# Kernel optimization log

Hardware: AMD Instinct MI355X
Metric: run time of the kernel (lower is better)

Reference implementation:

```python
import jax, jax.numpy as jnp
import numpy as np

B, NQ, C, H, W, HEADS = 8, 300, 256, 64, 64, 8
HD = C // HEADS
SCALING = float(HD) ** (-0.5)


def setup_inputs() -> dict:
    key = jax.random.key(0)
    ks = jax.random.split(key, 12)
    pts = jax.random.uniform(ks[3], (B, NQ, 2), jnp.float32)
    pts = pts * jnp.array([W - 1, H - 1], jnp.float32)  # (x, y) in pixel coords
    s = 1.0 / np.sqrt(C)
    return {
        "query": jax.random.normal(ks[0], (B, NQ, C), jnp.float32),
        "key": jax.random.normal(ks[1], (B, C, H, W), jnp.float32),
        "value": jax.random.normal(ks[2], (B, C, H, W), jnp.float32),
        "sampling_points": pts,
        "Wq": jax.random.normal(ks[4], (C, C), jnp.float32) * s,
        "bq": jnp.zeros((C,), jnp.float32),
        "Wk": jax.random.normal(ks[5], (C, C), jnp.float32) * s,
        "bk": jnp.zeros((C,), jnp.float32),
        "Wv": jax.random.normal(ks[6], (C, C), jnp.float32) * s,
        "bv": jnp.zeros((C,), jnp.float32),
        "Wo": jax.random.normal(ks[7], (C, C), jnp.float32) * s,
        "bo": jnp.zeros((C,), jnp.float32),
    }


def _sample_rows(feat, y):
    # feat: [b,heads,hd,h,w]; y: [b,q] float row coordinate.
    # Returns feat linearly interpolated in y for every column: [b,q,heads,hd,w]
    h = feat.shape[3]
    y0f = jnp.clip(jnp.floor(y), 0.0, h - 1)
    wy = y - y0f
    y0 = y0f.astype(jnp.int32)
    y1 = jnp.clip(y0 + 1, 0, h - 1)
    g = jax.vmap(lambda f, idx: f[:, :, idx, :])  # per-batch -> [heads,hd,q,w]
    r = g(feat, y0) * (1.0 - wy)[:, None, None, :, None] + g(feat, y1) * wy[:, None, None, :, None]
    return jnp.transpose(r, (0, 3, 1, 2, 4))


def _sample_cols(feat, x):
    # feat: [b,heads,hd,h,w]; x: [b,q] float col coordinate -> [b,q,heads,hd,h]
    w = feat.shape[4]
    x0f = jnp.clip(jnp.floor(x), 0.0, w - 1)
    wx = x - x0f
    x0 = x0f.astype(jnp.int32)
    x1 = jnp.clip(x0 + 1, 0, w - 1)
    g = jax.vmap(lambda f, idx: f[:, :, :, idx])  # per-batch -> [heads,hd,h,q]
    c = g(feat, x0) * (1.0 - wx)[:, None, None, None, :] + g(feat, x1) * wx[:, None, None, None, :]
    return jnp.transpose(c, (0, 4, 1, 2, 3))


def reference(query, key, value, sampling_points, Wq, bq, Wk, bk, Wv, bv, Wo, bo):
    b, nq, c = query.shape
    h, w = key.shape[2], key.shape[3]
    pq = (query @ Wq.T + bq) * SCALING                     # [b,nq,C]
    pk = jnp.einsum('oc,bchw->bohw', Wk, key) + bk[None, :, None, None]
    pv = jnp.einsum('oc,bchw->bohw', Wv, value) + bv[None, :, None, None]
    pq = pq.reshape(b, nq, HEADS, HD)
    pk = pk.reshape(b, HEADS, HD, h, w)
    pv = pv.reshape(b, HEADS, HD, h, w)
    x, y = sampling_points[..., 0], sampling_points[..., 1]
    # criss-cross weights: row through y (w samples) + column through x (h samples)
    k_row = _sample_rows(pk, y)                            # [b,q,heads,hd,w]
    k_col = _sample_cols(pk, x)                            # [b,q,heads,hd,h]
    w_row = jnp.einsum('bqnd,bqndw->bqnw', pq, k_row)
    w_col = jnp.einsum('bqnd,bqndk->bqnk', pq, k_col)
    attn = jax.nn.softmax(jnp.concatenate([w_row, w_col], axis=-1), axis=-1)
    a_row, a_col = attn[..., :w], attn[..., w:]
    v_row = _sample_rows(pv, y)
    v_col = _sample_cols(pv, x)
    out = jnp.einsum('bqnw,bqndw->bqnd', a_row, v_row) + jnp.einsum('bqnk,bqndk->bqnd', a_col, v_col)
    out = out.reshape(b, nq, c)
    return out @ Wo.T + bo
```

## Files before the change

kernel.cpp:

```cpp
#include <hip/hip_runtime.h>
#include <hip/hip_bf16.h>
#include <math.h>

constexpr int cB = 8, cNQ = 300, cC = 256, cH = 64, cW = 64, cHEADS = 8, cHD = 32;
constexpr int cHW = cH * cW;
constexpr int cM = cB * cNQ;
constexpr float cSCALE = 0.1767766952966369f;

typedef __bf16 bf16_t;
typedef bf16_t bf16x4 __attribute__((ext_vector_type(4)));
typedef bf16_t bf16x8 __attribute__((ext_vector_type(8)));
typedef float f32x4 __attribute__((ext_vector_type(4)));
typedef _Float16 f16_t;
typedef f16_t f16x8 __attribute__((ext_vector_type(8)));

__global__ __launch_bounds__(256) void proj_mfma_k(
    const float* __restrict__ X, const float* __restrict__ Wt,
    const float* __restrict__ bias, float* __restrict__ out,
    float scale, int M) {
  __shared__ bf16_t Xs[128 * 64];
  __shared__ bf16_t Ws[64 * 64];
  int m0 = blockIdx.x * 128;
  int o0 = blockIdx.y * 64;
  int tid = threadIdx.x;
  int lane = tid & 63, w = tid >> 6;
  int moff = (w & 1) * 64, ooff = (w >> 1) * 32;
  int l15 = lane & 15, l4 = lane >> 4;
  int srow = tid >> 1;
  int schalf = (tid & 1) * 32;
  int wo_l = tid >> 2;
  int wcg = (tid & 3) * 16;

  f32x4 acc[4][2];
#pragma unroll
  for (int m = 0; m < 4; ++m)
#pragma unroll
    for (int n = 0; n < 2; ++n) acc[m][n] = (f32x4){0.f, 0.f, 0.f, 0.f};

  for (int c0 = 0; c0 < cC; c0 += 64) {
    {
      int mrow = min(m0 + srow, M - 1);
      const float4* xr = (const float4*)(X + (size_t)mrow * cC + c0 + schalf);
      int sw = (srow & 7) * 8;
#pragma unroll
      for (int i = 0; i < 4; ++i) {
        float4 a = xr[i * 2], b4 = xr[i * 2 + 1];
        bf16x8 v = {(bf16_t)a.x, (bf16_t)a.y, (bf16_t)a.z, (bf16_t)a.w,
                    (bf16_t)b4.x, (bf16_t)b4.y, (bf16_t)b4.z, (bf16_t)b4.w};
        *(bf16x8*)&Xs[srow * 64 + ((schalf + i * 8) ^ sw)] = v;
      }
    }
    {
      const float4* wr = (const float4*)(Wt + (size_t)(o0 + wo_l) * cC + c0 + wcg);
      float4 a = wr[0], b4 = wr[1], c4 = wr[2], d4 = wr[3];
      bf16x8 w0 = {(bf16_t)a.x, (bf16_t)a.y, (bf16_t)a.z, (bf16_t)a.w,
                   (bf16_t)b4.x, (bf16_t)b4.y, (bf16_t)b4.z, (bf16_t)b4.w};
      bf16x8 w1 = {(bf16_t)c4.x, (bf16_t)c4.y, (bf16_t)c4.z, (bf16_t)c4.w,
                   (bf16_t)d4.x, (bf16_t)d4.y, (bf16_t)d4.z, (bf16_t)d4.w};
      int sw = (wo_l & 7) * 8;
      *(bf16x8*)&Ws[wo_l * 64 + (wcg ^ sw)] = w0;
      *(bf16x8*)&Ws[wo_l * 64 + ((wcg + 8) ^ sw)] = w1;
    }
    __syncthreads();
#pragma unroll
    for (int s = 0; s < 2; ++s) {
      int c8 = s * 32 + l4 * 8;
      bf16x8 afr[4], bfr[2];
#pragma unroll
      for (int m = 0; m < 4; ++m) {
        int r = moff + m * 16 + l15;
        afr[m] = *(const bf16x8*)&Xs[r * 64 + (c8 ^ ((r & 7) * 8))];
      }
#pragma unroll
      for (int n = 0; n < 2; ++n) {
        int r = ooff + n * 16 + l15;
        bfr[n] = *(const bf16x8*)&Ws[r * 64 + (c8 ^ ((r & 7) * 8))];
      }
#pragma unroll
      for (int m = 0; m < 4; ++m)
#pragma unroll
        for (int n = 0; n < 2; ++n)
          acc[m][n] = __builtin_amdgcn_mfma_f32_16x16x32_bf16(
              afr[m], bfr[n], acc[m][n], 0, 0, 0);
    }
    __syncthreads();
  }

  float b0 = bias[o0 + ooff + l15];
  float b1 = bias[o0 + ooff + 16 + l15];
#pragma unroll
  for (int m = 0; m < 4; ++m) {
    int mr = m0 + moff + m * 16 + l4 * 4;
#pragma unroll
    for (int reg = 0; reg < 4; ++reg) {
      if (mr + reg < M) {
        out[(size_t)(mr + reg) * cC + o0 + ooff + l15] =
            (acc[m][0][reg] + b0) * scale;
        out[(size_t)(mr + reg) * cC + o0 + ooff + 16 + l15] =
            (acc[m][1][reg] + b1) * scale;
      }
    }
  }
}

__global__ __launch_bounds__(256) void proj_kv_mfma_k(
    const float* __restrict__ key, const float* __restrict__ value,
    const float* __restrict__ Wk, const float* __restrict__ bk,
    const float* __restrict__ Wv, const float* __restrict__ bv,
    f16_t* __restrict__ pkT, f16_t* __restrict__ pvT,
    f16_t* __restrict__ pkTc, f16_t* __restrict__ pvTc) {
  int z = blockIdx.z;
  int b = z >> 1;
  bool isv = z & 1;
  const float* X = (isv ? value : key) + (size_t)b * cC * cHW;
  const float* Wm = isv ? Wv : Wk;
  const float* bb = isv ? bv : bk;
  f16_t* outT = (isv ? pvT : pkT) + (size_t)b * cHEADS * cHW * cHD;
  f16_t* outTc = (isv ? pvTc : pkTc) + (size_t)b * cHEADS * cHW * cHD;
  int hw0 = blockIdx.x * 128;
  int o0 = blockIdx.y * 64;

  __shared__ bf16_t Xs[128 * 64];
  __shared__ bf16_t Ws[64 * 64];

  int tid = threadIdx.x;
  int lane = tid & 63, w = tid >> 6;
  int hwl = (w & 1) * 64 + lane;
  int cbase = (w >> 1) * 32;
  int wo_l = tid >> 2;
  int wcg = (tid & 3) * 16;
  int hwoff = (w & 1) * 64, ooff = (w >> 1) * 32;
  int l15 = lane & 15, l4 = lane >> 4;

  f32x4 acc[4][2];
#pragma unroll
  for (int m = 0; m < 4; ++m)
#pragma unroll
    for (int n = 0; n < 2; ++n) acc[m][n] = (f32x4){0.f, 0.f, 0.f, 0.f};

  for (int c0 = 0; c0 < cC; c0 += 64) {
    const float* xcol = X + (size_t)(c0 + cbase) * cHW + hw0 + hwl;
#pragma unroll
    for (int i = 0; i < 8; ++i) {
      float f0 = xcol[(size_t)(i * 4 + 0) * cHW];
      float f1 = xcol[(size_t)(i * 4 + 1) * cHW];
      float f2 = xcol[(size_t)(i * 4 + 2) * cHW];
      float f3 = xcol[(size_t)(i * 4 + 3) * cHW];
      bf16x4 v = {(bf16_t)f0, (bf16_t)f1, (bf16_t)f2, (bf16_t)f3};
      int c_l = cbase + i * 4;
      *(bf16x4*)&Xs[hwl * 64 + (c_l ^ ((hwl & 7) * 8))] = v;
    }
    {
      const float4* wrow = (const float4*)(Wm + (size_t)(o0 + wo_l) * cC + c0 + wcg);
      float4 a = wrow[0], b4 = wrow[1], c4 = wrow[2], d4 = wrow[3];
      bf16x8 w0 = {(bf16_t)a.x, (bf16_t)a.y, (bf16_t)a.z, (bf16_t)a.w,
                   (bf16_t)b4.x, (bf16_t)b4.y, (bf16_t)b4.z, (bf16_t)b4.w};
      bf16x8 w1 = {(bf16_t)c4.x, (bf16_t)c4.y, (bf16_t)c4.z, (bf16_t)c4.w,
                   (bf16_t)d4.x, (bf16_t)d4.y, (bf16_t)d4.z, (bf16_t)d4.w};
      int sw = (wo_l & 7) * 8;
      *(bf16x8*)&Ws[wo_l * 64 + (wcg ^ sw)] = w0;
      *(bf16x8*)&Ws[wo_l * 64 + ((wcg + 8) ^ sw)] = w1;
    }
    __syncthreads();
#pragma unroll
    for (int s = 0; s < 2; ++s) {
      int c8 = s * 32 + l4 * 8;
      bf16x8 afr[4], bfr[2];
#pragma unroll
      for (int m = 0; m < 4; ++m) {
        int r = hwoff + m * 16 + l15;
        afr[m] = *(const bf16x8*)&Xs[r * 64 + (c8 ^ ((r & 7) * 8))];
      }
#pragma unroll
      for (int n = 0; n < 2; ++n) {
        int r = ooff + n * 16 + l15;
        bfr[n] = *(const bf16x8*)&Ws[r * 64 + (c8 ^ ((r & 7) * 8))];
      }
#pragma unroll
      for (int m = 0; m < 4; ++m)
#pragma unroll
        for (int n = 0; n < 2; ++n)
          acc[m][n] = __builtin_amdgcn_mfma_f32_16x16x32_bf16(
              afr[m], bfr[n], acc[m][n], 0, 0, 0);
    }
    __syncthreads();
  }

  int head = (o0 + ooff) >> 5;
  f16_t* obase = outT + (size_t)head * cHW * cHD;
  f16_t* obaseC = outTc + (size_t)head * cHW * cHD;
  float bias0 = bb[o0 + ooff + l15];
  float bias1 = bb[o0 + ooff + 16 + l15];
#pragma unroll
  for (int m = 0; m < 4; ++m) {
    int hwr = hwoff + m * 16 + l4 * 4;
#pragma unroll
    for (int reg = 0; reg < 4; ++reg) {
      int hw = hw0 + hwr + reg;
      f16_t v0 = (f16_t)(acc[m][0][reg] + bias0);
      f16_t v1 = (f16_t)(acc[m][1][reg] + bias1);
      size_t rowoff = (size_t)hw * cHD;
      obase[rowoff + l15] = v0;
      obase[rowoff + 16 + l15] = v1;
      int yy = hw >> 6, xx = hw & 63;
      size_t rowoffC = (size_t)(xx * cH + yy) * cHD;
      obaseC[rowoffC + l15] = v0;
      obaseC[rowoffC + 16 + l15] = v1;
    }
  }
}

__global__ __launch_bounds__(256) void attn_k(
    const float* __restrict__ pq, const f16_t* __restrict__ pkT,
    const f16_t* __restrict__ pkTc, const f16_t* __restrict__ pvT,
    const f16_t* __restrict__ pvTc, const float* __restrict__ pts,
    float* __restrict__ out) {
  int bid = blockIdx.x;
  int xcd = bid & 7;
  int t = bid >> 3;
  int phase = t / 150;
  int idx = t - phase * 150;
  int g = xcd + 8 * phase;
  int b = g >> 2;
  int hp = g & 3;
  int lane = threadIdx.x & 63;
  int wid = threadIdx.x >> 6;
  int n = hp * 2 + (wid & 1);
  int q = idx * 2 + (wid >> 1);

  float x = pts[((size_t)b * cNQ + q) * 2 + 0];
  float y = pts[((size_t)b * cNQ + q) * 2 + 1];
  float y0f = fminf(fmaxf(floorf(y), 0.f), (float)(cH - 1));
  float x0f = fminf(fmaxf(floorf(x), 0.f), (float)(cW - 1));
  float wy = y - y0f, wx = x - x0f;
  int y0 = (int)y0f, y1 = min(y0 + 1, cH - 1);
  int x0 = (int)x0f, x1 = min(x0 + 1, cW - 1);

  size_t hoff = (size_t)(b * cHEADS + n) * cHW * cHD;
  const f16_t* kTb = pkT + hoff;
  const f16_t* kTcb = pkTc + hoff;
  const f16_t* vTb = pvT + hoff;
  const f16_t* vTcb = pvTc + hoff;

  int g16 = lane >> 2, ch = lane & 3;
  f16x8 vr0[4], vr1[4], vc0[4], vc1[4];
#pragma unroll
  for (int k = 0; k < 4; ++k) {
    int p = g16 * 4 + k;
    vr0[k] = *(const f16x8*)(vTb + (size_t)(y0 * cW + p) * cHD + ch * 8);
    vr1[k] = *(const f16x8*)(vTb + (size_t)(y1 * cW + p) * cHD + ch * 8);
    vc0[k] = *(const f16x8*)(vTcb + (size_t)(x0 * cH + p) * cHD + ch * 8);
    vc1[k] = *(const f16x8*)(vTcb + (size_t)(x1 * cH + p) * cHD + ch * 8);
  }

  const f16x8* kr0 = (const f16x8*)(kTb + (size_t)(y0 * cW + lane) * cHD);
  const f16x8* kr1 = (const f16x8*)(kTb + (size_t)(y1 * cW + lane) * cHD);
  const f16x8* kc0 = (const f16x8*)(kTcb + (size_t)(x0 * cH + lane) * cHD);
  const f16x8* kc1 = (const f16x8*)(kTcb + (size_t)(x1 * cH + lane) * cHD);
  const float4* qb = (const float4*)(pq + ((size_t)b * cNQ + q) * cC + n * cHD);
  float wr0 = 0.f, wr1 = 0.f, wc0 = 0.f, wc1 = 0.f;
#pragma unroll
  for (int c = 0; c < 4; ++c) {
    f16x8 a0 = kr0[c], a1 = kr1[c], b0 = kc0[c], b1 = kc1[c];
    float4 q0 = qb[c * 2], q1 = qb[c * 2 + 1];
    float qs[8] = {q0.x, q0.y, q0.z, q0.w, q1.x, q1.y, q1.z, q1.w};
#pragma unroll
    for (int j = 0; j < 8; ++j) {
      float f0 = (float)a0[j], f1 = (float)a1[j];
      float h0 = (float)b0[j], h1 = (float)b1[j];
      if (j & 1) {
        wr1 += qs[j] * (f0 + wy * (f1 - f0));
        wc1 += qs[j] * (h0 + wx * (h1 - h0));
      } else {
        wr0 += qs[j] * (f0 + wy * (f1 - f0));
        wc0 += qs[j] * (h0 + wx * (h1 - h0));
      }
    }
  }
  float wrow = wr0 + wr1, wcol = wc0 + wc1;

  float m = fmaxf(wrow, wcol);
#pragma unroll
  for (int s = 32; s > 0; s >>= 1) m = fmaxf(m, __shfl_xor(m, s, 64));
  float er = expf(wrow - m), ec = expf(wcol - m);
  float ssum = er + ec;
#pragma unroll
  for (int s = 32; s > 0; s >>= 1) ssum += __shfl_xor(ssum, s, 64);

  float acc[8];
#pragma unroll
  for (int j = 0; j < 8; ++j) acc[j] = 0.f;
#pragma unroll
  for (int k = 0; k < 4; ++k) {
    int p = g16 * 4 + k;
    float ar = __shfl(er, p, 64);
    float ac = __shfl(ec, p, 64);
#pragma unroll
    for (int j = 0; j < 8; ++j) {
      float r0 = (float)vr0[k][j], r1 = (float)vr1[k][j];
      float c0 = (float)vc0[k][j], c1 = (float)vc1[k][j];
      acc[j] += ar * (r0 + wy * (r1 - r0)) + ac * (c0 + wx * (c1 - c0));
    }
  }
#pragma unroll
  for (int s = 4; s <= 32; s <<= 1)
#pragma unroll
    for (int j = 0; j < 8; ++j) acc[j] += __shfl_xor(acc[j], s, 64);

  float inv = 1.f / ssum;
  if (lane < 4) {
    float* op = out + ((size_t)b * cNQ + q) * cC + n * cHD + ch * 8;
    float4 o0 = {acc[0] * inv, acc[1] * inv, acc[2] * inv, acc[3] * inv};
    float4 o1 = {acc[4] * inv, acc[5] * inv, acc[6] * inv, acc[7] * inv};
    *(float4*)op = o0;
    *(float4*)(op + 4) = o1;
  }
}

extern "C" void kernel_launch(void* const* d_in, const int* in_sizes, int n_in,
                              void* d_out, int out_size, void* d_ws, size_t ws_size,
                              hipStream_t stream) {
  const float* query = (const float*)d_in[0];
  const float* key   = (const float*)d_in[1];
  const float* value = (const float*)d_in[2];
  const float* pts   = (const float*)d_in[3];
  const float* Wq = (const float*)d_in[4];
  const float* bq = (const float*)d_in[5];
  const float* Wk = (const float*)d_in[6];
  const float* bk = (const float*)d_in[7];
  const float* Wv = (const float*)d_in[8];
  const float* bv = (const float*)d_in[9];
  const float* Wo = (const float*)d_in[10];
  const float* bo = (const float*)d_in[11];
  float* out = (float*)d_out;

  const size_t kvsz = (size_t)cB * cC * cHW;
  float* pq = (float*)d_ws;
  f16_t* pkT = (f16_t*)(pq + (size_t)cM * cC);
  f16_t* pvT = pkT + kvsz;
  f16_t* pkTc = pvT + kvsz;
  f16_t* pvTc = pkTc + kvsz;
  float* ao = (float*)(pvTc + kvsz);

  proj_mfma_k<<<dim3((cM + 127) / 128, cC / 64), 256, 0, stream>>>(
      query, Wq, bq, pq, cSCALE, cM);
  proj_kv_mfma_k<<<dim3(cHW / 128, cC / 64, cB * 2), 256, 0, stream>>>(
      key, value, Wk, bk, Wv, bv, pkT, pvT, pkTc, pvTc);
  attn_k<<<cB * cNQ * 2, 256, 0, stream>>>(pq, pkT, pkTc, pvT, pvTc, pts, ao);
  proj_mfma_k<<<dim3((cM + 127) / 128, cC / 64), 256, 0, stream>>>(
      ao, Wo, bo, out, 1.0f, cM);
}
```

Measured before the change: 105.4 us.

## Load activations straight into MFMA fragments with register double-buffering

Both projection GEMM kernels stop staging activation tiles in LDS. Each lane now loads its own fp32 activation fragment from global memory directly into registers, converts it to bf16 and feeds it to MFMA, with two register buffers so the next k-step load overlaps the current MFMAs. Weights are pre-packed once per block into LDS in fragment order, which removes the per-k-step barriers. The cost is more registers and uncoalesced, strided global loads in the key/value kernel (16 lanes per channel row).

Measured after the change: 124.2 us. 17.8% more time.

```diff
diff --git a/kernel.cpp b/kernel.cpp
--- a/kernel.cpp
+++ b/kernel.cpp
@@ -8,7 +8,6 @@
 constexpr float cSCALE = 0.1767766952966369f;
 
 typedef __bf16 bf16_t;
-typedef bf16_t bf16x4 __attribute__((ext_vector_type(4)));
 typedef bf16_t bf16x8 __attribute__((ext_vector_type(8)));
 typedef float f32x4 __attribute__((ext_vector_type(4)));
 typedef _Float16 f16_t;
@@ -18,18 +17,33 @@
     const float* __restrict__ X, const float* __restrict__ Wt,
     const float* __restrict__ bias, float* __restrict__ out,
     float scale, int M) {
-  __shared__ bf16_t Xs[128 * 64];
-  __shared__ bf16_t Ws[64 * 64];
+  __shared__ bf16_t Wf[8 * 4 * 64 * 8];
   int m0 = blockIdx.x * 128;
   int o0 = blockIdx.y * 64;
   int tid = threadIdx.x;
   int lane = tid & 63, w = tid >> 6;
-  int moff = (w & 1) * 64, ooff = (w >> 1) * 32;
   int l15 = lane & 15, l4 = lane >> 4;
-  int srow = tid >> 1;
-  int schalf = (tid & 1) * 32;
-  int wo_l = tid >> 2;
-  int wcg = (tid & 3) * 16;
+
+  {
+    int ntile = tid >> 6;
+    int o = o0 + ntile * 16 + l15;
+    const float* wsrc = Wt + (size_t)o * cC + l4 * 8;
+#pragma unroll
+    for (int s = 0; s < 8; ++s) {
+      float4 f0 = *(const float4*)(wsrc + s * 32);
+      float4 f1 = *(const float4*)(wsrc + s * 32 + 4);
+      bf16x8 v = {(bf16_t)f0.x, (bf16_t)f0.y, (bf16_t)f0.z, (bf16_t)f0.w,
+                  (bf16_t)f1.x, (bf16_t)f1.y, (bf16_t)f1.z, (bf16_t)f1.w};
+      *(bf16x8*)&Wf[(size_t)((s * 4 + ntile) * 64 + lane) * 8] = v;
+    }
+  }
+  __syncthreads();
+
+  int moff = (w & 1) * 64;
+  int nbase = (w >> 1) * 2;
+  int mrow[4];
+#pragma unroll
+  for (int m = 0; m < 4; ++m) mrow[m] = min(m0 + moff + m * 16 + l15, M - 1);
 
   f32x4 acc[4][2];
 #pragma unroll
@@ -37,66 +51,51 @@
 #pragma unroll
     for (int n = 0; n < 2; ++n) acc[m][n] = (f32x4){0.f, 0.f, 0.f, 0.f};
 
-  for (int c0 = 0; c0 < cC; c0 += 64) {
-    {
-      int mrow = min(m0 + srow, M - 1);
-      const float4* xr = (const float4*)(X + (size_t)mrow * cC + c0 + schalf);
-      int sw = (srow & 7) * 8;
-#pragma unroll
-      for (int i = 0; i < 4; ++i) {
-        float4 a = xr[i * 2], b4 = xr[i * 2 + 1];
-        bf16x8 v = {(bf16_t)a.x, (bf16_t)a.y, (bf16_t)a.z, (bf16_t)a.w,
-                    (bf16_t)b4.x, (bf16_t)b4.y, (bf16_t)b4.z, (bf16_t)b4.w};
-        *(bf16x8*)&Xs[srow * 64 + ((schalf + i * 8) ^ sw)] = v;
-      }
-    }
-    {
-      const float4* wr = (const float4*)(Wt + (size_t)(o0 + wo_l) * cC + c0 + wcg);
-      float4 a = wr[0], b4 = wr[1], c4 = wr[2], d4 = wr[3];
-      bf16x8 w0 = {(bf16_t)a.x, (bf16_t)a.y, (bf16_t)a.z, (bf16_t)a.w,
-                   (bf16_t)b4.x, (bf16_t)b4.y, (bf16_t)b4.z, (bf16_t)b4.w};
-      bf16x8 w1 = {(bf16_t)c4.x, (bf16_t)c4.y, (bf16_t)c4.z, (bf16_t)c4.w,
-                   (bf16_t)d4.x, (bf16_t)d4.y, (bf16_t)d4.z, (bf16_t)d4.w};
-      int sw = (wo_l & 7) * 8;
-      *(bf16x8*)&Ws[wo_l * 64 + (wcg ^ sw)] = w0;
-      *(bf16x8*)&Ws[wo_l * 64 + ((wcg + 8) ^ sw)] = w1;
-    }
-    __syncthreads();
-#pragma unroll
-    for (int s = 0; s < 2; ++s) {
-      int c8 = s * 32 + l4 * 8;
-      bf16x8 afr[4], bfr[2];
-#pragma unroll
-      for (int m = 0; m < 4; ++m) {
-        int r = moff + m * 16 + l15;
-        afr[m] = *(const bf16x8*)&Xs[r * 64 + (c8 ^ ((r & 7) * 8))];
-      }
-#pragma unroll
-      for (int n = 0; n < 2; ++n) {
-        int r = ooff + n * 16 + l15;
-        bfr[n] = *(const bf16x8*)&Ws[r * 64 + (c8 ^ ((r & 7) * 8))];
-      }
-#pragma unroll
-      for (int m = 0; m < 4; ++m)
-#pragma unroll
-        for (int n = 0; n < 2; ++n)
-          acc[m][n] = __builtin_amdgcn_mfma_f32_16x16x32_bf16(
-              afr[m], bfr[n], acc[m][n], 0, 0, 0);
-    }
-    __syncthreads();
-  }
-
-  float b0 = bias[o0 + ooff + l15];
-  float b1 = bias[o0 + ooff + 16 + l15];
+  float4 fa[4][2], fb[4][2];
+  auto loadx = [&](float4 F[4][2], int s) {
+#pragma unroll
+    for (int m = 0; m < 4; ++m) {
+      const float4* xr = (const float4*)(X + (size_t)mrow[m] * cC + s * 32 + l4 * 8);
+      F[m][0] = xr[0];
+      F[m][1] = xr[1];
+    }
+  };
+  auto consume = [&](float4 F[4][2], int s) {
+    bf16x8 b0 = *(const bf16x8*)&Wf[(size_t)((s * 4 + nbase) * 64 + lane) * 8];
+    bf16x8 b1 = *(const bf16x8*)&Wf[(size_t)((s * 4 + nbase + 1) * 64 + lane) * 8];
+#pragma unroll
+    for (int m = 0; m < 4; ++m) {
+      float4 x0 = F[m][0], x1 = F[m][1];
+      bf16x8 a = {(bf16_t)x0.x, (bf16_t)x0.y, (bf16_t)x0.z, (bf16_t)x0.w,
+                  (bf16_t)x1.x, (bf16_t)x1.y, (bf16_t)x1.z, (bf16_t)x1.w};
+      acc[m][0] = __builtin_amdgcn_mfma_f32_16x16x32_bf16(a, b0, acc[m][0], 0, 0, 0);
+      acc[m][1] = __builtin_amdgcn_mfma_f32_16x16x32_bf16(a, b1, acc[m][1], 0, 0, 0);
+    }
+  };
+
+  loadx(fa, 0);
+#pragma unroll
+  for (int s = 0; s < 8; ++s) {
+    if (s & 1) {
+      if (s < 7) loadx(fa, s + 1);
+      consume(fb, s);
+    } else {
+      if (s < 7) loadx(fb, s + 1);
+      consume(fa, s);
+    }
+  }
+
+  float b0 = bias[o0 + nbase * 16 + l15];
+  float b1 = bias[o0 + nbase * 16 + 16 + l15];
 #pragma unroll
   for (int m = 0; m < 4; ++m) {
     int mr = m0 + moff + m * 16 + l4 * 4;
 #pragma unroll
     for (int reg = 0; reg < 4; ++reg) {
       if (mr + reg < M) {
-        out[(size_t)(mr + reg) * cC + o0 + ooff + l15] =
+        out[(size_t)(mr + reg) * cC + o0 + nbase * 16 + l15] =
             (acc[m][0][reg] + b0) * scale;
-        out[(size_t)(mr + reg) * cC + o0 + ooff + 16 + l15] =
+        out[(size_t)(mr + reg) * cC + o0 + nbase * 16 + 16 + l15] =
             (acc[m][1][reg] + b1) * scale;
       }
     }
@@ -120,77 +119,75 @@
   int hw0 = blockIdx.x * 128;
   int o0 = blockIdx.y * 64;
 
-  __shared__ bf16_t Xs[128 * 64];
-  __shared__ bf16_t Ws[64 * 64];
-
+  __shared__ bf16_t Wf[8 * 4 * 64 * 8];
   int tid = threadIdx.x;
   int lane = tid & 63, w = tid >> 6;
-  int hwl = (w & 1) * 64 + lane;
-  int cbase = (w >> 1) * 32;
-  int wo_l = tid >> 2;
-  int wcg = (tid & 3) * 16;
-  int hwoff = (w & 1) * 64, ooff = (w >> 1) * 32;
   int l15 = lane & 15, l4 = lane >> 4;
 
+  {
+    int ntile = tid >> 6;
+    int o = o0 + ntile * 16 + l15;
+    const float* wsrc = Wm + (size_t)o * cC + l4 * 8;
+#pragma unroll
+    for (int s = 0; s < 8; ++s) {
+      float4 f0 = *(const float4*)(wsrc + s * 32);
+      float4 f1 = *(const float4*)(wsrc + s * 32 + 4);
+      bf16x8 v = {(bf16_t)f0.x, (bf16_t)f0.y, (bf16_t)f0.z, (bf16_t)f0.w,
+                  (bf16_t)f1.x, (bf16_t)f1.y, (bf16_t)f1.z, (bf16_t)f1.w};
+      *(bf16x8*)&Wf[(size_t)((s * 4 + ntile) * 64 + lane) * 8] = v;
+    }
+  }
+  __syncthreads();
+
+  int hwoff = (w & 1) * 64;
+  int nbase = (w >> 1) * 2;
+  const float* xb = X + hw0 + hwoff + l15;
+
   f32x4 acc[4][2];
 #pragma unroll
   for (int m = 0; m < 4; ++m)
 #pragma unroll
     for (int n = 0; n < 2; ++n) acc[m][n] = (f32x4){0.f, 0.f, 0.f, 0.f};
 
-  for (int c0 = 0; c0 < cC; c0 += 64) {
-    const float* xcol = X + (size_t)(c0 + cbase) * cHW + hw0 + hwl;
-#pragma unroll
-    for (int i = 0; i < 8; ++i) {
-      float f0 = xcol[(size_t)(i * 4 + 0) * cHW];
-      float f1 = xcol[(size_t)(i * 4 + 1) * cHW];
-      float f2 = xcol[(size_t)(i * 4 + 2) * cHW];
-      float f3 = xcol[(size_t)(i * 4 + 3) * cHW];
-      bf16x4 v = {(bf16_t)f0, (bf16_t)f1, (bf16_t)f2, (bf16_t)f3};
-      int c_l = cbase + i * 4;
-      *(bf16x4*)&Xs[hwl * 64 + (c_l ^ ((hwl & 7) * 8))] = v;
-    }
-    {
-      const float4* wrow = (const float4*)(Wm + (size_t)(o0 + wo_l) * cC + c0 + wcg);
-      float4 a = wrow[0], b4 = wrow[1], c4 = wrow[2], d4 = wrow[3];
-      bf16x8 w0 = {(bf16_t)a.x, (bf16_t)a.y, (bf16_t)a.z, (bf16_t)a.w,
-                   (bf16_t)b4.x, (bf16_t)b4.y, (bf16_t)b4.z, (bf16_t)b4.w};
-      bf16x8 w1 = {(bf16_t)c4.x, (bf16_t)c4.y, (bf16_t)c4.z, (bf16_t)c4.w,
-                   (bf16_t)d4.x, (bf16_t)d4.y, (bf16_t)d4.z, (bf16_t)d4.w};
-      int sw = (wo_l & 7) * 8;
-      *(bf16x8*)&Ws[wo_l * 64 + (wcg ^ sw)] = w0;
-      *(bf16x8*)&Ws[wo_l * 64 + ((wcg + 8) ^ sw)] = w1;
-    }
-    __syncthreads();
-#pragma unroll
-    for (int s = 0; s < 2; ++s) {
-      int c8 = s * 32 + l4 * 8;
-      bf16x8 afr[4], bfr[2];
-#pragma unroll
-      for (int m = 0; m < 4; ++m) {
-        int r = hwoff + m * 16 + l15;
-        afr[m] = *(const bf16x8*)&Xs[r * 64 + (c8 ^ ((r & 7) * 8))];
-      }
-#pragma unroll
-      for (int n = 0; n < 2; ++n) {
-        int r = ooff + n * 16 + l15;
-        bfr[n] = *(const bf16x8*)&Ws[r * 64 + (c8 ^ ((r & 7) * 8))];
-      }
-#pragma unroll
-      for (int m = 0; m < 4; ++m)
-#pragma unroll
-        for (int n = 0; n < 2; ++n)
-          acc[m][n] = __builtin_amdgcn_mfma_f32_16x16x32_bf16(
-              afr[m], bfr[n], acc[m][n], 0, 0, 0);
-    }
-    __syncthreads();
-  }
-
-  int head = (o0 + ooff) >> 5;
+  float fa[4][8], fb[4][8];
+  auto loadx = [&](float F[4][8], int s) {
+    const float* xc = xb + (size_t)(s * 32 + l4 * 8) * cHW;
+#pragma unroll
+    for (int m = 0; m < 4; ++m)
+#pragma unroll
+      for (int j = 0; j < 8; ++j)
+        F[m][j] = xc[(size_t)j * cHW + m * 16];
+  };
+  auto consume = [&](float F[4][8], int s) {
+    bf16x8 b0 = *(const bf16x8*)&Wf[(size_t)((s * 4 + nbase) * 64 + lane) * 8];
+    bf16x8 b1 = *(const bf16x8*)&Wf[(size_t)((s * 4 + nbase + 1) * 64 + lane) * 8];
+#pragma unroll
+    for (int m = 0; m < 4; ++m) {
+      bf16x8 a = {(bf16_t)F[m][0], (bf16_t)F[m][1], (bf16_t)F[m][2],
+                  (bf16_t)F[m][3], (bf16_t)F[m][4], (bf16_t)F[m][5],
+                  (bf16_t)F[m][6], (bf16_t)F[m][7]};
+      acc[m][0] = __builtin_amdgcn_mfma_f32_16x16x32_bf16(a, b0, acc[m][0], 0, 0, 0);
+      acc[m][1] = __builtin_amdgcn_mfma_f32_16x16x32_bf16(a, b1, acc[m][1], 0, 0, 0);
+    }
+  };
+
+  loadx(fa, 0);
+#pragma unroll
+  for (int s = 0; s < 8; ++s) {
+    if (s & 1) {
+      if (s < 7) loadx(fa, s + 1);
+      consume(fb, s);
+    } else {
+      if (s < 7) loadx(fb, s + 1);
+      consume(fa, s);
+    }
+  }
+
+  int head = (o0 + nbase * 16) >> 5;
   f16_t* obase = outT + (size_t)head * cHW * cHD;
   f16_t* obaseC = outTc + (size_t)head * cHW * cHD;
-  float bias0 = bb[o0 + ooff + l15];
-  float bias1 = bb[o0 + ooff + 16 + l15];
+  float bias0 = bb[o0 + nbase * 16 + l15];
+  float bias1 = bb[o0 + nbase * 16 + 16 + l15];
 #pragma unroll
   for (int m = 0; m < 4; ++m) {
     int hwr = hwoff + m * 16 + l4 * 4;
```

## Double-buffer LDS and register-prefetch next K tile in KV projection GEMM

Applied to the files above, without the earlier changes.

Reworks the key/value projection GEMM to prefetch the next 64-channel slice of X and W into registers while the current slice is consumed. LDS is double-buffered, which removes one barrier per K step. Weights are now stored in LDS directly in MFMA fragment order, so B-fragment reads are contiguous with no swizzle. The cost is higher register pressure (32 floats plus 4 float4 held per thread) and double the shared memory, which may lower occupancy.

Result: slower. 108.8 us (+3.2%).

```diff
diff --git a/kernel.cpp b/kernel.cpp
--- a/kernel.cpp
+++ b/kernel.cpp
@@ -120,17 +120,19 @@
   int hw0 = blockIdx.x * 128;
   int o0 = blockIdx.y * 64;
 
-  __shared__ bf16_t Xs[128 * 64];
-  __shared__ bf16_t Ws[64 * 64];
+  __shared__ bf16_t Xs[2][128 * 64];
+  __shared__ bf16_t Wf[2][2 * 4 * 64 * 8];
 
   int tid = threadIdx.x;
   int lane = tid & 63, w = tid >> 6;
+  int l15 = lane & 15, l4 = lane >> 4;
   int hwl = (w & 1) * 64 + lane;
   int cbase = (w >> 1) * 32;
-  int wo_l = tid >> 2;
-  int wcg = (tid & 3) * 16;
-  int hwoff = (w & 1) * 64, ooff = (w >> 1) * 32;
-  int l15 = lane & 15, l4 = lane >> 4;
+  int hwoff = (w & 1) * 64;
+  int nbase = (w >> 1) * 2;
+
+  const float* xbase = X + hw0 + hwl;
+  const float* wbase = Wm + (size_t)(o0 + w * 16 + l15) * cC + l4 * 8;
 
   f32x4 acc[4][2];
 #pragma unroll
@@ -138,59 +140,61 @@
 #pragma unroll
     for (int n = 0; n < 2; ++n) acc[m][n] = (f32x4){0.f, 0.f, 0.f, 0.f};
 
-  for (int c0 = 0; c0 < cC; c0 += 64) {
-    const float* xcol = X + (size_t)(c0 + cbase) * cHW + hw0 + hwl;
+  float xr[32];
+  float4 wr[4];
+
+  auto issue = [&](int c0) {
+#pragma unroll
+    for (int i = 0; i < 32; ++i)
+      xr[i] = xbase[(size_t)(c0 + cbase + i) * cHW];
+#pragma unroll
+    for (int ks = 0; ks < 2; ++ks) {
+      const float4* p = (const float4*)(wbase + c0 + ks * 32);
+      wr[ks * 2] = p[0];
+      wr[ks * 2 + 1] = p[1];
+    }
+  };
+
+  issue(0);
+#pragma unroll
+  for (int s = 0; s < 4; ++s) {
+    const int buf = s & 1;
 #pragma unroll
     for (int i = 0; i < 8; ++i) {
-      float f0 = xcol[(size_t)(i * 4 + 0) * cHW];
-      float f1 = xcol[(size_t)(i * 4 + 1) * cHW];
-      float f2 = xcol[(size_t)(i * 4 + 2) * cHW];
-      float f3 = xcol[(size_t)(i * 4 + 3) * cHW];
-      bf16x4 v = {(bf16_t)f0, (bf16_t)f1, (bf16_t)f2, (bf16_t)f3};
+      bf16x4 v = {(bf16_t)xr[i * 4 + 0], (bf16_t)xr[i * 4 + 1],
+                  (bf16_t)xr[i * 4 + 2], (bf16_t)xr[i * 4 + 3]};
       int c_l = cbase + i * 4;
-      *(bf16x4*)&Xs[hwl * 64 + (c_l ^ ((hwl & 7) * 8))] = v;
-    }
-    {
-      const float4* wrow = (const float4*)(Wm + (size_t)(o0 + wo_l) * cC + c0 + wcg);
-      float4 a = wrow[0], b4 = wrow[1], c4 = wrow[2], d4 = wrow[3];
-      bf16x8 w0 = {(bf16_t)a.x, (bf16_t)a.y, (bf16_t)a.z, (bf16_t)a.w,
-                   (bf16_t)b4.x, (bf16_t)b4.y, (bf16_t)b4.z, (bf16_t)b4.w};
-      bf16x8 w1 = {(bf16_t)c4.x, (bf16_t)c4.y, (bf16_t)c4.z, (bf16_t)c4.w,
-                   (bf16_t)d4.x, (bf16_t)d4.y, (bf16_t)d4.z, (bf16_t)d4.w};
-      int sw = (wo_l & 7) * 8;
-      *(bf16x8*)&Ws[wo_l * 64 + (wcg ^ sw)] = w0;
-      *(bf16x8*)&Ws[wo_l * 64 + ((wcg + 8) ^ sw)] = w1;
-    }
+      *(bf16x4*)&Xs[buf][hwl * 64 + (c_l ^ ((hwl & 7) * 8))] = v;
+    }
+#pragma unroll
+    for (int ks = 0; ks < 2; ++ks) {
+      float4 a = wr[ks * 2], b4 = wr[ks * 2 + 1];
+      bf16x8 v = {(bf16_t)a.x, (bf16_t)a.y, (bf16_t)a.z, (bf16_t)a.w,
+                  (bf16_t)b4.x, (bf16_t)b4.y, (bf16_t)b4.z, (bf16_t)b4.w};
+      *(bf16x8*)&Wf[buf][(size_t)((ks * 4 + w) * 64 + lane) * 8] = v;
+    }
+    if (s < 3) issue((s + 1) * 64);
     __syncthreads();
 #pragma unroll
-    for (int s = 0; s < 2; ++s) {
-      int c8 = s * 32 + l4 * 8;
-      bf16x8 afr[4], bfr[2];
+    for (int ks = 0; ks < 2; ++ks) {
+      int c8 = ks * 32 + l4 * 8;
+      bf16x8 bfr0 = *(const bf16x8*)&Wf[buf][(size_t)((ks * 4 + nbase) * 64 + lane) * 8];
+      bf16x8 bfr1 = *(const bf16x8*)&Wf[buf][(size_t)((ks * 4 + nbase + 1) * 64 + lane) * 8];
 #pragma unroll
       for (int m = 0; m < 4; ++m) {
         int r = hwoff + m * 16 + l15;
-        afr[m] = *(const bf16x8*)&Xs[r * 64 + (c8 ^ ((r & 7) * 8))];
-      }
-#pragma unroll
-      for (int n = 0; n < 2; ++n) {
-        int r = ooff + n * 16 + l15;
-        bfr[n] = *(const bf16x8*)&Ws[r * 64 + (c8 ^ ((r & 7) * 8))];
-      }
-#pragma unroll
-      for (int m = 0; m < 4; ++m)
-#pragma unroll
-        for (int n = 0; n < 2; ++n)
-          acc[m][n] = __builtin_amdgcn_mfma_f32_16x16x32_bf16(
-              afr[m], bfr[n], acc[m][n], 0, 0, 0);
-    }
-    __syncthreads();
-  }
-
-  int head = (o0 + ooff) >> 5;
+        bf16x8 a = *(const bf16x8*)&Xs[buf][r * 64 + (c8 ^ ((r & 7) * 8))];
+        acc[m][0] = __builtin_amdgcn_mfma_f32_16x16x32_bf16(a, bfr0, acc[m][0], 0, 0, 0);
+        acc[m][1] = __builtin_amdgcn_mfma_f32_16x16x32_bf16(a, bfr1, acc[m][1], 0, 0, 0);
+      }
+    }
+  }
+
+  int head = (o0 + nbase * 16) >> 5;
   f16_t* obase = outT + (size_t)head * cHW * cHD;
   f16_t* obaseC = outTc + (size_t)head * cHW * cHD;
-  float bias0 = bb[o0 + ooff + l15];
-  float bias1 = bb[o0 + ooff + 16 + l15];
+  float bias0 = bb[o0 + nbase * 16 + l15];
+  float bias1 = bb[o0 + nbase * 16 + 16 + l15];
 #pragma unroll
   for (int m = 0; m < 4; ++m) {
     int hwr = hwoff + m * 16 + l4 * 4;
```
